# Performance work log

Measured on AMD Instinct MI355X. Metric: run time of the kernel, lower is better.

## Reference

```python
import jax, jax.numpy as jnp
import numpy as np
from jax import lax

B, T, F = 128, 100, 64
HID = [16, 32]  # encoder hidden dims; decoder uses reversed [32, 16]
K = 3


def _conv2d(x, w, b):
    # x: [N, Cin, H, W], w: [Cout, Cin, kh, kw] -> 'SAME' padding as in torch padding=k//2
    y = lax.conv_general_dilated(x, w, (1, 1), 'SAME',
                                 dimension_numbers=('NCHW', 'OIHW', 'NCHW'))
    return y + b[None, :, None, None]


def _convlstm_layer(xs, w, b, h0, c0):
    # xs: [T, B, Cin, H, W] time-major; returns hidden seq [T,B,Chid,H,W] and final (h, c)
    def step(carry, x_t):
        h, c = carry
        z = _conv2d(jnp.concatenate([x_t, h], axis=1), w, b)
        i, f, o, g = jnp.split(z, 4, axis=1)  # gate order i, f, o, g
        c2 = jax.nn.sigmoid(f) * c + jax.nn.sigmoid(i) * jnp.tanh(g)
        h2 = jax.nn.sigmoid(o) * jnp.tanh(c2)
        return (h2, c2), h2
    (hT, cT), hs = lax.scan(step, (h0, c0), xs)
    return hs, (hT, cT)


def setup_inputs() -> dict:
    key = jax.random.key(0)
    ks = jax.random.split(key, 12)
    s = 0.05
    inp = {
        'x': jax.random.normal(ks[0], (B, T, F), dtype=jnp.float32),
        # encoder layer 0: in=1+16, out=4*16
        'enc_w0': jax.random.normal(ks[1], (4 * HID[0], 1 + HID[0], K, K), dtype=jnp.float32) * s,
        'enc_b0': jnp.zeros((4 * HID[0],), dtype=jnp.float32),
        # encoder layer 1: in=16+32, out=4*32
        'enc_w1': jax.random.normal(ks[2], (4 * HID[1], HID[0] + HID[1], K, K), dtype=jnp.float32) * s,
        'enc_b1': jnp.zeros((4 * HID[1],), dtype=jnp.float32),
        # decoder layer 0: hidden=32, input=32 (last encoder hidden)
        'dec_w0': jax.random.normal(ks[3], (4 * HID[1], HID[1] + HID[1], K, K), dtype=jnp.float32) * s,
        'dec_b0': jnp.zeros((4 * HID[1],), dtype=jnp.float32),
        # decoder layer 1: hidden=16, input=32
        'dec_w1': jax.random.normal(ks[4], (4 * HID[0], HID[1] + HID[0], K, K), dtype=jnp.float32) * s,
        'dec_b1': jnp.zeros((4 * HID[0],), dtype=jnp.float32),
        # final 1x1 conv: 16 -> 1
        'fc_w': jax.random.normal(ks[5], (1, HID[0], 1, 1), dtype=jnp.float32) * s,
        'fc_b': jnp.zeros((1,), dtype=jnp.float32),
    }
    return inp


def reference(x, enc_w0, enc_b0, enc_w1, enc_b1, dec_w0, dec_b0, dec_w1, dec_b1, fc_w, fc_b):
    b, t, f = x.shape
    # [b,t,f] -> [t,b,1,f,1] time-major, spatial (f,1)
    xs = jnp.transpose(x.reshape(b, t, 1, f, 1), (1, 0, 2, 3, 4))
    z16 = jnp.zeros((b, HID[0], f, 1), x.dtype)
    z32 = jnp.zeros((b, HID[1], f, 1), x.dtype)

    enc1, (h1, c1) = _convlstm_layer(xs, enc_w0, enc_b0, z16, z16)
    enc2, (h2, c2) = _convlstm_layer(enc1, enc_w1, enc_b1, z32, z32)

    # decoder initial states = encoder final states reversed
    dec1, _ = _convlstm_layer(enc2, dec_w0, dec_b0, h2, c2)
    dec2, _ = _convlstm_layer(dec1, dec_w1, dec_b1, h1, c1)  # [t,b,16,f,1]

    # final 1x1 conv applied per timestep == one batched conv over t*b
    flat = dec2.reshape(t * b, HID[0], f, 1)
    out = _conv2d(flat, fc_w, fc_b)  # [t*b,1,f,1]
    recon = jnp.transpose(out.reshape(t, b, f), (1, 0, 2))  # [b,t,f]
    return recon
```

## Files before the change

### kernel.cpp

```cpp
#include <hip/hip_runtime.h>
#include <math.h>

#define B_ 128
#define T_ 100
#define RS 72
#define RS2 40

__device__ __forceinline__ float frcp_(float x){ return __builtin_amdgcn_rcpf(x); }
__device__ __forceinline__ float fsig_(float x){ return frcp_(1.f + __expf(-x)); }
__device__ __forceinline__ float ftanh_(float x){ float e = __expf(2.f*x); return 1.f - 2.f*frcp_(e+1.f); }
__device__ __forceinline__ float gate1(float zi, float zf, float zo, float zg, float& c){
    float cc = fsig_(zf)*c + fsig_(zi)*ftanh_(zg);
    c = cc;
    return fsig_(zo)*ftanh_(cc);
}
__device__ __forceinline__ float4 ldf4(const float* p){ return *reinterpret_cast<const float4*>(p); }
__device__ __forceinline__ void stf4(float* p, float4 v){ *reinterpret_cast<float4*>(p) = v; }
__device__ __forceinline__ float2 ldf2(const float* p){ return *reinterpret_cast<const float2*>(p); }
__device__ __forceinline__ void stf2(float* p, float2 v){ *reinterpret_cast<float2*>(p) = v; }
__device__ __forceinline__ float4 add4(float4 a, float4 b){
    return make_float4(a.x+b.x, a.y+b.y, a.z+b.z, a.w+b.w);
}
__device__ __forceinline__ float4 gate4(float4 zi, float4 zf, float4 zo, float4 zg,
                                        float bi, float bf, float bo, float bg, float4& c){
    float4 h;
    h.x = gate1(zi.x+bi, zf.x+bf, zo.x+bo, zg.x+bg, c.x);
    h.y = gate1(zi.y+bi, zf.y+bf, zo.y+bo, zg.y+bg, c.y);
    h.z = gate1(zi.z+bi, zf.z+bf, zo.z+bo, zg.z+bg, c.z);
    h.w = gate1(zi.w+bi, zf.w+bf, zo.w+bo, zg.w+bg, c.w);
    return h;
}

__device__ __forceinline__ void fma4v(float w, float u0,float u1,float u2,float u3, float4& a){
    a.x = fmaf(w,u0,a.x); a.y = fmaf(w,u1,a.y);
    a.z = fmaf(w,u2,a.z); a.w = fmaf(w,u3,a.w);
}
__device__ __forceinline__ void fma2v(float w, float u0,float u1, float2& a){
    a.x = fmaf(w,u0,a.x); a.y = fmaf(w,u1,a.y);
}

template<int ROWS>
__device__ __forceinline__ void rowacc4(const float* __restrict__ rowp,
                                        const float* __restrict__ wk,
                                        float4& ai, float4& af, float4& ao, float4& ag)
{
    float  m = rowp[-1];
    float4 a = ldf4(rowp);
    float  p = rowp[4];
    float4 wa = ldf4(wk);
    float4 wb = ldf4(wk + ROWS);
    float4 wc = ldf4(wk + 2*ROWS);
    fma4v(wa.x, m,a.x,a.y,a.z, ai);  fma4v(wa.y, m,a.x,a.y,a.z, af);
    fma4v(wa.z, m,a.x,a.y,a.z, ao);  fma4v(wa.w, m,a.x,a.y,a.z, ag);
    fma4v(wb.x, a.x,a.y,a.z,a.w, ai); fma4v(wb.y, a.x,a.y,a.z,a.w, af);
    fma4v(wb.z, a.x,a.y,a.z,a.w, ao); fma4v(wb.w, a.x,a.y,a.z,a.w, ag);
    fma4v(wc.x, a.y,a.z,a.w,p, ai);  fma4v(wc.y, a.y,a.z,a.w,p, af);
    fma4v(wc.z, a.y,a.z,a.w,p, ao);  fma4v(wc.w, a.y,a.z,a.w,p, ag);
}
template<int ROWS>
__device__ __forceinline__ void rowacc2(const float* __restrict__ rowp,
                                        const float* __restrict__ wk,
                                        float2& ai, float2& af, float2& ao, float2& ag)
{
    float  m = rowp[-1];
    float2 a = *reinterpret_cast<const float2*>(rowp);
    float  p = rowp[2];
    float4 wa = ldf4(wk);
    float4 wb = ldf4(wk + ROWS);
    float4 wc = ldf4(wk + 2*ROWS);
    fma2v(wa.x, m,a.x, ai); fma2v(wa.y, m,a.x, af);
    fma2v(wa.z, m,a.x, ao); fma2v(wa.w, m,a.x, ag);
    fma2v(wb.x, a.x,a.y, ai); fma2v(wb.y, a.x,a.y, af);
    fma2v(wb.z, a.x,a.y, ao); fma2v(wb.w, a.x,a.y, ag);
    fma2v(wc.x, a.y,p, ai); fma2v(wc.y, a.y,p, af);
    fma2v(wc.z, a.y,p, ao); fma2v(wc.w, a.y,p, ag);
}
template<int ROWS>
__device__ __forceinline__ void rowacc8(const float* __restrict__ rowp,
                                        const float* __restrict__ wk,
                                        float4& i0, float4& i1, float4& f0v, float4& f1v,
                                        float4& o0, float4& o1, float4& g0, float4& g1)
{
    float  m = rowp[-1];
    float4 a = ldf4(rowp);
    float4 b = ldf4(rowp + 4);
    float  p = rowp[8];
    float4 wa = ldf4(wk);
    float4 wb = ldf4(wk + ROWS);
    float4 wc = ldf4(wk + 2*ROWS);
    fma4v(wa.x, m,a.x,a.y,a.z, i0);   fma4v(wa.x, a.w,b.x,b.y,b.z, i1);
    fma4v(wa.y, m,a.x,a.y,a.z, f0v);  fma4v(wa.y, a.w,b.x,b.y,b.z, f1v);
    fma4v(wa.z, m,a.x,a.y,a.z, o0);   fma4v(wa.z, a.w,b.x,b.y,b.z, o1);
    fma4v(wa.w, m,a.x,a.y,a.z, g0);   fma4v(wa.w, a.w,b.x,b.y,b.z, g1);
    fma4v(wb.x, a.x,a.y,a.z,a.w, i0); fma4v(wb.x, b.x,b.y,b.z,b.w, i1);
    fma4v(wb.y, a.x,a.y,a.z,a.w, f0v);fma4v(wb.y, b.x,b.y,b.z,b.w, f1v);
    fma4v(wb.z, a.x,a.y,a.z,a.w, o0); fma4v(wb.z, b.x,b.y,b.z,b.w, o1);
    fma4v(wb.w, a.x,a.y,a.z,a.w, g0); fma4v(wb.w, b.x,b.y,b.z,b.w, g1);
    fma4v(wc.x, a.y,a.z,a.w,b.x, i0); fma4v(wc.x, b.y,b.z,b.w,p, i1);
    fma4v(wc.y, a.y,a.z,a.w,b.x, f0v);fma4v(wc.y, b.y,b.z,b.w,p, f1v);
    fma4v(wc.z, a.y,a.z,a.w,b.x, o0); fma4v(wc.z, b.y,b.z,b.w,p, o1);
    fma4v(wc.w, a.y,a.z,a.w,b.x, g0); fma4v(wc.w, b.y,b.z,b.w,p, g1);
}

__global__ __launch_bounds__(512, 1) void enc_kernel(
    const float* __restrict__ x,
    const float* __restrict__ w0, const float* __restrict__ b0,
    const float* __restrict__ w1, const float* __restrict__ b1,
    float* __restrict__ seq,
    float* __restrict__ h1f, float* __restrict__ c1f,
    float* __restrict__ h2f, float* __restrict__ c2f,
    float* __restrict__ comm, int* __restrict__ flags)
{
    __shared__ float wl0[51 * 64];
    __shared__ float wl1[144 * 128];
    __shared__ float bs0[64];
    __shared__ float bs1[128];
    __shared__ float hbuf[50 * RS2];
    __shared__ float zsA[4 * 16 * 32];
    __shared__ float zsB[4 * 32 * 32];

    const int tid = threadIdx.x;
    const int b = blockIdx.x & 127;
    const int s = blockIdx.x >> 7;
    const int gofs = s << 5;
    const int kg = tid >> 8;
    const int r  = tid & 255;
    const int chB = r >> 3, f0B = (r & 7) * 4;
    const int chA = r >> 4, f0A = (r & 15) * 2;
    const int haloSlot = s ? 3 : 36;
    const int myId = (b << 1) | s;
    const int peerId = myId ^ 1;
    float* mySend = &comm[(size_t)myId * 128];
    const float* peerBuf = &comm[(size_t)peerId * 128];

    for (int idx = tid; idx < 51 * 64; idx += 512) {
        int k = idx >> 6, rr = idx & 63;
        int ch = rr >> 2, g = rr & 3;
        int ci = k / 3, d = k - ci * 3;
        wl0[idx] = w0[((g * 16 + ch) * 17 + ci) * 9 + d * 3 + 1];
    }
    for (int idx = tid; idx < 144 * 128; idx += 512) {
        int k = idx >> 7, rr = idx & 127;
        int ch = rr >> 2, g = rr & 3;
        int ci = k / 3, d = k - ci * 3;
        wl1[idx] = w1[((g * 32 + ch) * 48 + ci) * 9 + d * 3 + 1];
    }
    if (tid < 64) bs0[tid] = b0[tid];
    if (tid < 128) bs1[tid] = b1[tid];
    for (int i = tid; i < 50 * RS2; i += 512) hbuf[i] = 0.f;
    __syncthreads();

    const int xl = tid - 256;
    if (xl >= 0 && xl < 34) {
        const int gc = gofs - 1 + xl;
        const bool v = (gc >= 0) && (gc < 64);
        hbuf[0 * RS2 + 3 + xl] = v ? x[(b * T_ + 0) * 64 + gc] : 0.f;
        hbuf[1 * RS2 + 3 + xl] = v ? x[(b * T_ + 1) * 64 + gc] : 0.f;
    }
    const float biA = bs0[chA], bfA = bs0[16+chA], boA = bs0[32+chA], bgA = bs0[48+chA];
    const float biB = bs1[chB], bfB = bs1[32+chB], boB = bs1[64+chB], bgB = bs1[96+chB];
    __syncthreads();

    const float4 z4 = make_float4(0.f, 0.f, 0.f, 0.f);
    const float2 z2 = make_float2(0.f, 0.f);
    float2 c0q = z2;
    float4 c1a = z4;

    if (kg == 0) {
        float2 ai = z2, af = z2, ao = z2, ag = z2;
        rowacc2<64>(&hbuf[0 * RS2 + 4 + f0A], &wl0[chA * 4], ai, af, ao, ag);
        float2 hq;
        hq.x = gate1(ai.x + biA, af.x + bfA, ao.x + boA, ag.x + bgA, c0q.x);
        hq.y = gate1(ai.y + biA, af.y + bfA, ao.y + boA, ag.y + bgA, c0q.y);
        *reinterpret_cast<float2*>(&hbuf[(2 + chA) * RS2 + 4 + f0A]) = hq;
        if ((r & 15) == (s ? 0 : 15)) {
            const float v = s ? hq.x : hq.y;
            __hip_atomic_store((unsigned int*)&mySend[1 * 64 + 32 + chA],
                               __float_as_uint(v),
                               __ATOMIC_RELAXED, __HIP_MEMORY_SCOPE_AGENT);
        }
    }
    __syncthreads();

#pragma unroll 1
    for (int t = 0; t < T_; ++t) {
        if (tid == 0)
            __hip_atomic_store(&flags[myId], t + 1,
                               __ATOMIC_RELAXED, __HIP_MEMORY_SCOPE_AGENT);
        if (tid < 48 && (t > 0 || tid >= 32)) {
            while (__hip_atomic_load(&flags[peerId],
                                     __ATOMIC_ACQUIRE, __HIP_MEMORY_SCOPE_AGENT) < t + 1)
                __builtin_amdgcn_s_sleep(2);
            const int par = (t + 1) & 1;
            const unsigned int uv =
                __hip_atomic_load((const unsigned int*)&peerBuf[par * 64 + tid],
                                  __ATOMIC_RELAXED, __HIP_MEMORY_SCOPE_AGENT);
            const float v = __uint_as_float(uv);
            if (tid < 32) hbuf[(18 + tid) * RS2 + haloSlot] = v;
            else          hbuf[(2 + (tid - 32)) * RS2 + haloSlot] = v;
        }
        __syncthreads();

        const bool doL0 = (t + 1 < T_);
        float4 I = z4, F = z4, O = z4, G = z4;
#pragma unroll 1
        for (int j = 0; j < 24; ++j) {
            const int ci = kg * 24 + j;
            rowacc4<128>(&hbuf[(2 + ci) * RS2 + 4 + f0B],
                         &wl1[(ci * 3) * 128 + chB * 4], I, F, O, G);
        }
        float2 ai = z2, af = z2, ao = z2, ag = z2;
        if (doL0) {
            if (kg == 0) {
                rowacc2<64>(&hbuf[((t + 1) & 1) * RS2 + 4 + f0A], &wl0[chA * 4],
                            ai, af, ao, ag);
#pragma unroll 1
                for (int j = 0; j < 8; ++j)
                    rowacc2<64>(&hbuf[(2 + j) * RS2 + 4 + f0A],
                                &wl0[((1 + j) * 3) * 64 + chA * 4], ai, af, ao, ag);
            } else {
#pragma unroll 1
                for (int j = 8; j < 16; ++j)
                    rowacc2<64>(&hbuf[(2 + j) * RS2 + 4 + f0A],
                                &wl0[((1 + j) * 3) * 64 + chA * 4], ai, af, ao, ag);
            }
        }
        if (kg == 1) {
            stf4(&zsB[(0*32+chB)*32 + f0B], I);
            stf4(&zsB[(1*32+chB)*32 + f0B], F);
            stf4(&zsB[(2*32+chB)*32 + f0B], O);
            stf4(&zsB[(3*32+chB)*32 + f0B], G);
            if (doL0) {
                *reinterpret_cast<float2*>(&zsA[(0*16+chA)*32 + f0A]) = ai;
                *reinterpret_cast<float2*>(&zsA[(1*16+chA)*32 + f0A]) = af;
                *reinterpret_cast<float2*>(&zsA[(2*16+chA)*32 + f0A]) = ao;
                *reinterpret_cast<float2*>(&zsA[(3*16+chA)*32 + f0A]) = ag;
            }
            if (xl >= 0 && xl < 34 && t + 2 < T_) {
                const int gc = gofs - 1 + xl;
                hbuf[(t & 1) * RS2 + 3 + xl] =
                    (gc >= 0 && gc < 64) ? x[(b * T_ + t + 2) * 64 + gc] : 0.f;
            }
        }
        __syncthreads();
        if (kg == 0) {
            float4 zi = add4(I, ldf4(&zsB[(0*32+chB)*32 + f0B]));
            float4 zf = add4(F, ldf4(&zsB[(1*32+chB)*32 + f0B]));
            float4 zo = add4(O, ldf4(&zsB[(2*32+chB)*32 + f0B]));
            float4 zg = add4(G, ldf4(&zsB[(3*32+chB)*32 + f0B]));
            float4 hq = gate4(zi, zf, zo, zg, biB, bfB, boB, bgB, c1a);
            stf4(&hbuf[(18 + chB) * RS2 + 4 + f0B], hq);
            stf4(&seq[((size_t)t * B_ + b) * 2048 + chB * 64 + gofs + f0B], hq);
            if (doL0 && (r & 7) == (s ? 0 : 7)) {
                const float v = s ? hq.x : hq.w;
                __hip_atomic_store((unsigned int*)&mySend[(t & 1) * 64 + chB],
                                   __float_as_uint(v),
                                   __ATOMIC_RELAXED, __HIP_MEMORY_SCOPE_AGENT);
            }
            if (doL0) {
                float2 pzi = *reinterpret_cast<const float2*>(&zsA[(0*16+chA)*32 + f0A]);
                float2 pzf = *reinterpret_cast<const float2*>(&zsA[(1*16+chA)*32 + f0A]);
                float2 pzo = *reinterpret_cast<const float2*>(&zsA[(2*16+chA)*32 + f0A]);
                float2 pzg = *reinterpret_cast<const float2*>(&zsA[(3*16+chA)*32 + f0A]);
                float2 hq2;
                hq2.x = gate1(ai.x+pzi.x+biA, af.x+pzf.x+bfA, ao.x+pzo.x+boA, ag.x+pzg.x+bgA, c0q.x);
                hq2.y = gate1(ai.y+pzi.y+biA, af.y+pzf.y+bfA, ao.y+pzo.y+boA, ag.y+pzg.y+bgA, c0q.y);
                *reinterpret_cast<float2*>(&hbuf[(2 + chA) * RS2 + 4 + f0A]) = hq2;
                if ((r & 15) == (s ? 0 : 15)) {
                    const float v = s ? hq2.x : hq2.y;
                    __hip_atomic_store((unsigned int*)&mySend[(t & 1) * 64 + 32 + chA],
                                       __float_as_uint(v),
                                       __ATOMIC_RELAXED, __HIP_MEMORY_SCOPE_AGENT);
                }
            }
        }
        __syncthreads();
    }

    if (kg == 0) {
        *reinterpret_cast<float2*>(&h1f[(b * 16 + chA) * 64 + gofs + f0A]) =
            *reinterpret_cast<const float2*>(&hbuf[(2 + chA) * RS2 + 4 + f0A]);
        *reinterpret_cast<float2*>(&c1f[(b * 16 + chA) * 64 + gofs + f0A]) = c0q;
        stf4(&h2f[b * 2048 + chB * 64 + gofs + f0B],
             ldf4(&hbuf[(18 + chB) * RS2 + 4 + f0B]));
        stf4(&c2f[b * 2048 + chB * 64 + gofs + f0B], c1a);
    }
}

__global__ __launch_bounds__(256, 2) void xconv0_kernel(
    const float* __restrict__ seqIn, const float* __restrict__ w,
    float* __restrict__ zx, int t0)
{
    __shared__ float wl[96 * 128];
    __shared__ float xt[32 * RS];

    const int tid = threadIdx.x;
    const int tl = blockIdx.x / B_;
    const int b  = blockIdx.x - tl * B_;
    const int t  = t0 + tl;

    for (int idx = tid; idx < 96 * 128; idx += 256) {
        int k = idx >> 7, rr = idx & 127;
        int ch = rr >> 2, g = rr & 3;
        int ci = k / 3, d = k - ci * 3;
        wl[idx] = w[((g * 32 + ch) * 64 + ci) * 9 + d * 3 + 1];
    }
    {
        int rr = tid >> 3, j = tid & 7;
        xt[rr * RS + (j < 4 ? j : 64 + j)] = 0.f;
    }
    {
        const float* s = &seqIn[((size_t)t * B_ + b) * 2048 + tid * 8];
        float4 v0 = ldf4(s);
        float4 v1 = ldf4(s + 4);
        int ci = tid >> 3, col = (tid & 7) * 8;
        stf4(&xt[ci * RS + 4 + col], v0);
        stf4(&xt[ci * RS + 4 + col + 4], v1);
    }
    __syncthreads();

    const int ch = tid >> 3, f0 = (tid & 7) * 8;
    const float4 z4 = make_float4(0.f,0.f,0.f,0.f);
    float4 i0=z4,i1=z4,f0v=z4,f1v=z4,o0=z4,o1=z4,g0=z4,g1=z4;
#pragma unroll 1
    for (int rr = 0; rr < 32; ++rr)
        rowacc8<128>(&xt[rr * RS + 4 + f0], wl + (rr * 3) * 128 + ch * 4,
                     i0, i1, f0v, f1v, o0, o1, g0, g1);

    float* zp = &zx[(((size_t)tl * B_ + b) * 4) * 2048 + ch * 64 + f0];
    stf4(zp, i0);            stf4(zp + 4, i1);
    stf4(zp + 2048, f0v);    stf4(zp + 2048 + 4, f1v);
    stf4(zp + 4096, o0);     stf4(zp + 4096 + 4, o1);
    stf4(zp + 6144, g0);     stf4(zp + 6144 + 4, g1);
}

__global__ __launch_bounds__(512, 1) void decg(
    const float* __restrict__ w0, const float* __restrict__ b0,
    const float* __restrict__ w1, const float* __restrict__ b1,
    const float* __restrict__ zx,
    const float* __restrict__ h0in, const float* __restrict__ c0in,
    const float* __restrict__ h1in, const float* __restrict__ c1in,
    float* __restrict__ h0sv, float* __restrict__ c0sv,
    float* __restrict__ h1sv, float* __restrict__ c1sv,
    const float* __restrict__ fw, const float* __restrict__ fb,
    float* __restrict__ out,
    float* __restrict__ comm0, float* __restrict__ comm1,
    int* __restrict__ flg, int t0, int tn, int lastc)
{
    __shared__ float wl0[96 * 128];
    __shared__ float wl1[144 * 64];
    __shared__ float hp0[32 * RS2];
    __shared__ float hp1[16 * RS2];
    __shared__ float zs0[4 * 32 * 32];
    __shared__ float zs1[4 * 16 * 32];
    __shared__ float bs0[128];
    __shared__ float bs1[64];
    __shared__ float fcw[16];
    __shared__ float fcb_s;

    const int tid = threadIdx.x;
    const int b = blockIdx.x & 127;
    const int s = blockIdx.x >> 7;
    const int gofs = s << 5;
    const int haloSlot = s ? 3 : 36;
    const int bcol = s ? 31 : 32;
    const int myId = (b << 1) | s, peerId = myId ^ 1;
    float* send0 = &comm0[(size_t)myId * 64];
    const float* peer0 = &comm0[(size_t)peerId * 64];
    float* send1 = &comm1[(size_t)myId * 32];
    const float* peer1 = &comm1[(size_t)peerId * 32];

    const int kg = tid >> 8;
    const int r = tid & 255;
    const bool isD0 = (r < 128);
    const int ch0 = r >> 2, t0f = (r & 3) * 8;
    const int r1 = r - 128;
    const int ch1 = r1 >> 3, t1f = (r1 & 7) * 4;

    for (int idx = tid; idx < 96 * 128; idx += 512) {
        int k = idx >> 7, rr = idx & 127;
        int c8 = rr >> 2, g = rr & 3;
        int ci = k / 3, d = k - ci * 3;
        wl0[idx] = w0[((g * 32 + c8) * 64 + 32 + ci) * 9 + d * 3 + 1];
    }
    for (int idx = tid; idx < 144 * 64; idx += 512) {
        int k = idx >> 6, rr = idx & 63;
        int c8 = rr >> 2, g = rr & 3;
        int ci = k / 3, d = k - ci * 3;
        wl1[idx] = w1[((g * 16 + c8) * 48 + ci) * 9 + d * 3 + 1];
    }
    if (tid < 128) bs0[tid] = b0[tid];
    if (tid < 64) bs1[tid] = b1[tid];
    if (tid < 16) fcw[tid] = fw[tid];
    if (tid == 16) fcb_s = fb[0];
    for (int i = tid; i < 32 * RS2; i += 512) hp0[i] = 0.f;
    for (int i = tid; i < 16 * RS2; i += 512) hp1[i] = 0.f;
    __syncthreads();

    for (int i = tid; i < 1024; i += 512) {
        int c8 = i >> 5, f = i & 31;
        hp0[c8 * RS2 + 4 + f] = h0in[b * 2048 + c8 * 64 + gofs + f];
    }
    { int c8 = tid >> 5, f = tid & 31;
      hp1[c8 * RS2 + 4 + f] = h1in[b * 1024 + c8 * 64 + gofs + f]; }
    if (tid < 32) hp0[tid * RS2 + haloSlot] = h0in[b * 2048 + tid * 64 + bcol];
    if (tid >= 64 && tid < 80)
        hp1[(tid - 64) * RS2 + haloSlot] = h1in[b * 1024 + (tid - 64) * 64 + bcol];

    const float4 z4 = make_float4(0.f, 0.f, 0.f, 0.f);
    float4 c0a = z4, c0b = z4;
    float4 c1v = z4;
    float bi, bfv, bo, bg;
    if (isD0) { bi = bs0[ch0]; bfv = bs0[32+ch0]; bo = bs0[64+ch0]; bg = bs0[96+ch0]; }
    else      { bi = bs1[ch1]; bfv = bs1[16+ch1]; bo = bs1[32+ch1]; bg = bs1[48+ch1]; }
    if (kg == 0) {
        if (isD0) {
            c0a = ldf4(&c0in[b * 2048 + ch0 * 64 + gofs + t0f]);
            c0b = ldf4(&c0in[b * 2048 + ch0 * 64 + gofs + t0f + 4]);
        } else {
            c1v = ldf4(&c1in[b * 1024 + ch1 * 64 + gofs + t1f]);
        }
    }
    const float fcbv = fcb_s;

#pragma unroll 1
    for (int u = t0; u < t0 + tn + lastc; ++u) {
        if (tid == 0)
            __hip_atomic_store(&flg[myId], u,
                               __ATOMIC_RELAXED, __HIP_MEMORY_SCOPE_AGENT);
        if (u > t0) {
            const int par = (u - 1) & 1;
            if (tid < 32) {
                while (__hip_atomic_load(&flg[peerId],
                                         __ATOMIC_ACQUIRE, __HIP_MEMORY_SCOPE_AGENT) < u)
                    __builtin_amdgcn_s_sleep(2);
                hp0[tid * RS2 + haloSlot] = __uint_as_float(
                    __hip_atomic_load((const unsigned int*)&peer0[par * 32 + tid],
                                      __ATOMIC_RELAXED, __HIP_MEMORY_SCOPE_AGENT));
            } else if (tid >= 64 && tid < 80 && u >= 2) {
                while (__hip_atomic_load(&flg[peerId],
                                         __ATOMIC_ACQUIRE, __HIP_MEMORY_SCOPE_AGENT) < u)
                    __builtin_amdgcn_s_sleep(2);
                hp1[(tid - 64) * RS2 + haloSlot] = __uint_as_float(
                    __hip_atomic_load((const unsigned int*)&peer1[par * 16 + (tid - 64)],
                                      __ATOMIC_RELAXED, __HIP_MEMORY_SCOPE_AGENT));
            }
        }
        __syncthreads();

        const bool d0act = (u - t0 < tn);
        const bool d1act = (u >= 1);
        float4 A0=z4,A1=z4,B0=z4,B1=z4,C0=z4,C1=z4,D0=z4,D1=z4;
        float4 ai=z4, af=z4, ao=z4, ag=z4;
        float4 X0=z4,X1=z4,X2=z4,X3=z4,X4=z4,X5=z4,X6=z4,X7=z4;

        if (isD0) {
            if (d0act) {
                if (kg == 0) {
                    const float* zp = &zx[(((size_t)(u - t0) * B_ + b) * 4) * 2048
                                          + ch0 * 64 + gofs + t0f];
                    X0 = ldf4(zp);         X1 = ldf4(zp + 4);
                    X2 = ldf4(zp + 2048);  X3 = ldf4(zp + 2052);
                    X4 = ldf4(zp + 4096);  X5 = ldf4(zp + 4100);
                    X6 = ldf4(zp + 6144);  X7 = ldf4(zp + 6148);
                }
#pragma unroll 1
                for (int j = 0; j < 16; ++j) {
                    const int ci = kg * 16 + j;
                    rowacc8<128>(&hp0[ci * RS2 + 4 + t0f], &wl0[(ci * 3) * 128 + ch0 * 4],
                                 A0, A1, B0, B1, C0, C1, D0, D1);
                }
            }
            if (kg == 1 && r < 32 && u >= 2) {
                float a = fcbv;
#pragma unroll
                for (int k2 = 0; k2 < 16; ++k2)
                    a = fmaf(fcw[k2], hp1[k2 * RS2 + 4 + r], a);
                out[(b * T_ + (u - 2)) * 64 + gofs + r] = a;
            }
        } else if (d1act) {
            if (kg == 0) {
#pragma unroll 1
                for (int j = 0; j < 24; ++j)
                    rowacc4<64>(&hp0[j * RS2 + 4 + t1f], &wl1[(j * 3) * 64 + ch1 * 4],
                                ai, af, ao, ag);
            } else {
#pragma unroll 1
                for (int j = 24; j < 32; ++j)
                    rowacc4<64>(&hp0[j * RS2 + 4 + t1f], &wl1[(j * 3) * 64 + ch1 * 4],
                                ai, af, ao, ag);
#pragma unroll 1
                for (int j = 0; j < 16; ++j)
                    rowacc4<64>(&hp1[j * RS2 + 4 + t1f], &wl1[((32 + j) * 3) * 64 + ch1 * 4],
                                ai, af, ao, ag);
            }
        }
        if (kg == 1) {
            if (isD0) { if (d0act) {
                stf4(&zs0[(0*32+ch0)*32 + t0f], A0); stf4(&zs0[(0*32+ch0)*32 + t0f + 4], A1);
                stf4(&zs0[(1*32+ch0)*32 + t0f], B0); stf4(&zs0[(1*32+ch0)*32 + t0f + 4], B1);
                stf4(&zs0[(2*32+ch0)*32 + t0f], C0); stf4(&zs0[(2*32+ch0)*32 + t0f + 4], C1);
                stf4(&zs0[(3*32+ch0)*32 + t0f], D0); stf4(&zs0[(3*32+ch0)*32 + t0f + 4], D1);
            }} else { if (d1act) {
                stf4(&zs1[(0*16+ch1)*32 + t1f], ai);
                stf4(&zs1[(1*16+ch1)*32 + t1f], af);
                stf4(&zs1[(2*16+ch1)*32 + t1f], ao);
                stf4(&zs1[(3*16+ch1)*32 + t1f], ag);
            }}
        }
        __syncthreads();
        if (kg == 0) {
            if (isD0 && d0act) {
                float4 zi0 = add4(add4(A0, X0), ldf4(&zs0[(0*32+ch0)*32 + t0f]));
                float4 zi1 = add4(add4(A1, X1), ldf4(&zs0[(0*32+ch0)*32 + t0f + 4]));
                float4 zf0 = add4(add4(B0, X2), ldf4(&zs0[(1*32+ch0)*32 + t0f]));
                float4 zf1 = add4(add4(B1, X3), ldf4(&zs0[(1*32+ch0)*32 + t0f + 4]));
                float4 zo0 = add4(add4(C0, X4), ldf4(&zs0[(2*32+ch0)*32 + t0f]));
                float4 zo1 = add4(add4(C1, X5), ldf4(&zs0[(2*32+ch0)*32 + t0f + 4]));
                float4 zg0 = add4(add4(D0, X6), ldf4(&zs0[(3*32+ch0)*32 + t0f]));
                float4 zg1 = add4(add4(D1, X7), ldf4(&zs0[(3*32+ch0)*32 + t0f + 4]));
                float4 h0q0 = gate4(zi0, zf0, zo0, zg0, bi, bfv, bo, bg, c0a);
                float4 h0q1 = gate4(zi1, zf1, zo1, zg1, bi, bfv, bo, bg, c0b);
                stf4(&hp0[ch0 * RS2 + 4 + t0f], h0q0);
                stf4(&hp0[ch0 * RS2 + 4 + t0f + 4], h0q1);
                if ((r & 3) == (s ? 0 : 3)) {
                    __hip_atomic_store((unsigned int*)&send0[(u & 1) * 32 + ch0],
                                       __float_as_uint(s ? h0q0.x : h0q1.w),
                                       __ATOMIC_RELAXED, __HIP_MEMORY_SCOPE_AGENT);
                }
            } else if (!isD0 && d1act) {
                float4 zi = add4(ai, ldf4(&zs1[(0*16+ch1)*32 + t1f]));
                float4 zf = add4(af, ldf4(&zs1[(1*16+ch1)*32 + t1f]));
                float4 zo = add4(ao, ldf4(&zs1[(2*16+ch1)*32 + t1f]));
                float4 zg = add4(ag, ldf4(&zs1[(3*16+ch1)*32 + t1f]));
                float4 h1q = gate4(zi, zf, zo, zg, bi, bfv, bo, bg, c1v);
                stf4(&hp1[ch1 * RS2 + 4 + t1f], h1q);
                if ((r1 & 7) == (s ? 0 : 7)) {
                    __hip_atomic_store((unsigned int*)&send1[(u & 1) * 16 + ch1],
                                       __float_as_uint(s ? h1q.x : h1q.w),
                                       __ATOMIC_RELAXED, __HIP_MEMORY_SCOPE_AGENT);
                }
            }
        }
        __syncthreads();
    }

    if (lastc && tid < 32) {
        float a = fcbv;
#pragma unroll
        for (int k2 = 0; k2 < 16; ++k2)
            a = fmaf(fcw[k2], hp1[k2 * RS2 + 4 + tid], a);
        out[(b * T_ + (T_ - 1)) * 64 + gofs + tid] = a;
    }
    for (int i = tid; i < 1024; i += 512) {
        int c8 = i >> 5, f = i & 31;
        h0sv[b * 2048 + c8 * 64 + gofs + f] = hp0[c8 * RS2 + 4 + f];
    }
    { int c8 = tid >> 5, f = tid & 31;
      h1sv[b * 1024 + c8 * 64 + gofs + f] = hp1[c8 * RS2 + 4 + f]; }
    if (kg == 0) {
        if (isD0) {
            stf4(&c0sv[b * 2048 + ch0 * 64 + gofs + t0f], c0a);
            stf4(&c0sv[b * 2048 + ch0 * 64 + gofs + t0f + 4], c0b);
        } else {
            stf4(&c1sv[b * 1024 + ch1 * 64 + gofs + t1f], c1v);
        }
    }
}

__global__ __launch_bounds__(512, 1) void dec0_fb(
    const float* __restrict__ w, const float* __restrict__ bias,
    float* __restrict__ seq,
    const float* __restrict__ hin, const float* __restrict__ cin)
{
    __shared__ float wl[192 * 128];
    __shared__ float bs[128];
    __shared__ float xin[32 * RS];
    __shared__ float hp[32 * RS];

    const int tid = threadIdx.x;
    const int b = blockIdx.x;

    for (int idx = tid; idx < 192 * 128; idx += 512) {
        int k = idx >> 7, rr = idx & 127;
        int ch = rr >> 2, g = rr & 3;
        int ci = k / 3, d = k - ci * 3;
        wl[idx] = w[((g * 32 + ch) * 64 + ci) * 9 + d * 3 + 1];
    }
    if (tid < 128) bs[tid] = bias[tid];
    for (int i = tid; i < 32 * RS; i += 512) { xin[i] = 0.f; hp[i] = 0.f; }
    __syncthreads();
    {
        const float* hs = &hin[b * 2048 + tid * 4];
        float4 hv = ldf4(hs);
        int ci = tid >> 4, col = (tid & 15) * 4;
        stf4(&hp[ci * RS + 4 + col], hv);
    }
    const int ch = tid >> 4, f0 = (tid & 15) * 4;
    float4 cc = ldf4(&cin[b * 2048 + ch * 64 + f0]);
    const float bi = bs[ch], bf = bs[32 + ch], bo = bs[64 + ch], bg = bs[96 + ch];
    const float4 z4 = make_float4(0.f,0.f,0.f,0.f);

    float4 nx = ldf4(&seq[(size_t)b * 2048 + tid * 4]);

#pragma unroll 1
    for (int t = 0; t < T_; ++t) {
        {
            int ci = tid >> 4, col = (tid & 15) * 4;
            stf4(&xin[ci * RS + 4 + col], nx);
        }
        __syncthreads();
        if (t + 1 < T_)
            nx = ldf4(&seq[((size_t)(t + 1) * B_ + b) * 2048 + tid * 4]);
        float4 ai = z4, af = z4, ao = z4, ag = z4;
#pragma unroll 1
        for (int rr = 0; rr < 32; ++rr)
            rowacc4<128>(&xin[rr * RS + 4 + f0], wl + (rr * 3) * 128 + ch * 4, ai, af, ao, ag);
#pragma unroll 1
        for (int rr = 0; rr < 32; ++rr)
            rowacc4<128>(&hp[rr * RS + 4 + f0], wl + ((32 + rr) * 3) * 128 + ch * 4, ai, af, ao, ag);
        float4 hn = gate4(ai, af, ao, ag, bi, bf, bo, bg, cc);
        __syncthreads();
        stf4(&hp[ch * RS + 4 + f0], hn);
        stf4(&seq[((size_t)t * B_ + b) * 2048 + ch * 64 + f0], hn);
    }
}

__global__ __launch_bounds__(512, 1) void dec1_fb(
    const float* __restrict__ w, const float* __restrict__ bias,
    const float* __restrict__ seq,
    const float* __restrict__ hin, const float* __restrict__ cin,
    const float* __restrict__ fw, const float* __restrict__ fb,
    float* __restrict__ out)
{
    __shared__ float wl[144 * 64];
    __shared__ float bs[64];
    __shared__ float xin[32 * RS];
    __shared__ float hp[16 * RS];
    __shared__ float fcw[16];
    __shared__ float fcb;

    const int tid = threadIdx.x;
    const int b = blockIdx.x;

    for (int idx = tid; idx < 144 * 64; idx += 512) {
        int k = idx >> 6, rr = idx & 63;
        int ch = rr >> 2, g = rr & 3;
        int ci = k / 3, d = k - ci * 3;
        wl[idx] = w[((g * 16 + ch) * 48 + ci) * 9 + d * 3 + 1];
    }
    if (tid < 64) bs[tid] = bias[tid];
    if (tid < 16) fcw[tid] = fw[tid];
    if (tid == 16) fcb = fb[0];
    for (int i = tid; i < 32 * RS; i += 512) xin[i] = 0.f;
    for (int i = tid; i < 16 * RS; i += 512) hp[i] = 0.f;
    __syncthreads();
    {
        const float* hs = &hin[b * 1024 + tid * 2];
        float2 hv = *reinterpret_cast<const float2*>(hs);
        int ci = tid >> 5, col = (tid & 31) * 2;
        *reinterpret_cast<float2*>(&hp[ci * RS + 4 + col]) = hv;
    }
    const int ch = tid >> 5, f0 = (tid & 31) * 2;
    float2 cc = *reinterpret_cast<const float2*>(&cin[b * 1024 + ch * 64 + f0]);
    const float bi = bs[ch], bf = bs[16 + ch], bo = bs[32 + ch], bg = bs[48 + ch];
    const float2 z2 = make_float2(0.f,0.f);
    float4 nx = ldf4(&seq[(size_t)b * 2048 + tid * 4]);
    __syncthreads();

#pragma unroll 1
    for (int t = 0; t < T_; ++t) {
        {
            int ci = tid >> 4, col = (tid & 15) * 4;
            stf4(&xin[ci * RS + 4 + col], nx);
        }
        __syncthreads();
        if (t + 1 < T_)
            nx = ldf4(&seq[((size_t)(t + 1) * B_ + b) * 2048 + tid * 4]);

        float2 ai = z2, af = z2, ao = z2, ag = z2;
#pragma unroll 1
        for (int rr = 0; rr < 32; ++rr)
            rowacc2<64>(&xin[rr * RS + 4 + f0], wl + (rr * 3) * 64 + ch * 4, ai, af, ao, ag);
#pragma unroll 1
        for (int rr = 0; rr < 16; ++rr)
            rowacc2<64>(&hp[rr * RS + 4 + f0], wl + ((32 + rr) * 3) * 64 + ch * 4, ai, af, ao, ag);

        float2 hh;
        hh.x = gate1(ai.x + bi, af.x + bf, ao.x + bo, ag.x + bg, cc.x);
        hh.y = gate1(ai.y + bi, af.y + bf, ao.y + bo, ag.y + bg, cc.y);
        __syncthreads();
        *reinterpret_cast<float2*>(&hp[ch * RS + 4 + f0]) = hh;
        __syncthreads();

        if (tid < 64) {
            float a = fcb;
#pragma unroll
            for (int k2 = 0; k2 < 16; ++k2)
                a = fmaf(fcw[k2], hp[k2 * RS + 4 + tid], a);
            out[(b * T_ + t) * 64 + tid] = a;
        }
    }
}

extern "C" void kernel_launch(void* const* d_in, const int* in_sizes, int n_in,
                              void* d_out, int out_size, void* d_ws, size_t ws_size,
                              hipStream_t stream)
{
    (void)in_sizes; (void)n_in; (void)out_size;
    const float* x   = (const float*)d_in[0];
    const float* ew0 = (const float*)d_in[1];
    const float* eb0 = (const float*)d_in[2];
    const float* ew1 = (const float*)d_in[3];
    const float* eb1 = (const float*)d_in[4];
    const float* dw0 = (const float*)d_in[5];
    const float* db0 = (const float*)d_in[6];
    const float* dw1 = (const float*)d_in[7];
    const float* db1 = (const float*)d_in[8];
    const float* fw  = (const float*)d_in[9];
    const float* fb  = (const float*)d_in[10];
    float* out = (float*)d_out;

    float* ws  = (float*)d_ws;
    size_t off = 0;
    float* seq = ws + off; off += (size_t)T_ * B_ * 2048;
    float* h1f = ws + off; off += (size_t)B_ * 1024;
    float* c1f = ws + off; off += (size_t)B_ * 1024;
    float* h2f = ws + off; off += (size_t)B_ * 2048;
    float* c2f = ws + off; off += (size_t)B_ * 2048;
    float* hd0 = ws + off; off += (size_t)B_ * 2048;
    float* cd0 = ws + off; off += (size_t)B_ * 2048;
    float* hd1 = ws + off; off += (size_t)B_ * 1024;
    float* cd1 = ws + off; off += (size_t)B_ * 1024;
    float* comm = ws + off; off += 32768 + 16384 + 8192;
    int*   flg  = (int*)(ws + off); off += 1024;
    float* zx  = ws + off;

    float* commD0 = comm + 32768;
    float* commD1 = comm + 32768 + 16384;

    size_t availf = (ws_size / 4 > off) ? (ws_size / 4 - off) : 0;
    int TC = 0;
    if      (availf >= (size_t)100 * B_ * 8192) TC = 100;
    else if (availf >= (size_t)50  * B_ * 8192) TC = 50;
    else if (availf >= (size_t)25  * B_ * 8192) TC = 25;
    else if (availf >= (size_t)10  * B_ * 8192) TC = 10;

    hipMemsetAsync(flg, 0, 512 * sizeof(int), stream);
    enc_kernel<<<256, 512, 0, stream>>>(x, ew0, eb0, ew1, eb1, seq,
                                        h1f, c1f, h2f, c2f, comm, flg);

    if (TC > 0) {
        for (int t0 = 0; t0 < T_; t0 += TC) {
            int tn = (t0 + TC <= T_) ? TC : (T_ - t0);
            int lastc = (t0 + tn >= T_) ? 1 : 0;
            xconv0_kernel<<<tn * B_, 256, 0, stream>>>(seq, dw0, zx, t0);
            decg<<<256, 512, 0, stream>>>(
                dw0, db0, dw1, db1, zx,
                t0 == 0 ? h2f : hd0, t0 == 0 ? c2f : cd0,
                t0 == 0 ? h1f : hd1, t0 == 0 ? c1f : cd1,
                hd0, cd0, hd1, cd1,
                fw, fb, out, commD0, commD1, flg + 256, t0, tn, lastc);
        }
    } else {
        dec0_fb<<<B_, 512, 0, stream>>>(dw0, db0, seq, h2f, c2f);
        dec1_fb<<<B_, 512, 0, stream>>>(dw1, db1, seq, h1f, c1f, fw, fb, out);
    }
}
```

Before: 2.066 ms.

## Repartition encoder layer-1 and decoder layer-1 convs into four-way input-channel split-K

The encoder's second ConvLSTM layer previously split its 48 input rows between two 256-thread halves, each thread computing 4 columns. It now splits them four ways across 128-thread groups, each thread computing 8 columns with rowacc8. Three partial sums go to a larger shared buffer and group 0 reduces them and applies the gates. The decoder layer-1 work gets the same treatment: its 48 input rows are split evenly into four 12-row chunks instead of an uneven 24/24 split. The aim is to shorten the serial per-timestep critical path and improve per-thread reuse, at the cost of more shared memory, extra reduction loads and higher register pressure.

```diff
diff --git a/kernel.cpp b/kernel.cpp
--- a/kernel.cpp
+++ b/kernel.cpp
@@ -117,7 +117,7 @@
     __shared__ float bs1[128];
     __shared__ float hbuf[50 * RS2];
     __shared__ float zsA[4 * 16 * 32];
-    __shared__ float zsB[4 * 32 * 32];
+    __shared__ float zsB3[3 * 4096];
 
     const int tid = threadIdx.x;
     const int b = blockIdx.x & 127;
@@ -125,7 +125,9 @@
     const int gofs = s << 5;
     const int kg = tid >> 8;
     const int r  = tid & 255;
-    const int chB = r >> 3, f0B = (r & 7) * 4;
+    const int g  = tid >> 7;
+    const int rg = tid & 127;
+    const int chB = rg >> 2, f0B = (rg & 3) * 8;
     const int chA = r >> 4, f0A = (r & 15) * 2;
     const int haloSlot = s ? 3 : 36;
     const int myId = (b << 1) | s;
@@ -135,15 +137,15 @@
 
     for (int idx = tid; idx < 51 * 64; idx += 512) {
         int k = idx >> 6, rr = idx & 63;
-        int ch = rr >> 2, g = rr & 3;
+        int ch = rr >> 2, gg = rr & 3;
         int ci = k / 3, d = k - ci * 3;
-        wl0[idx] = w0[((g * 16 + ch) * 17 + ci) * 9 + d * 3 + 1];
+        wl0[idx] = w0[((gg * 16 + ch) * 17 + ci) * 9 + d * 3 + 1];
     }
     for (int idx = tid; idx < 144 * 128; idx += 512) {
         int k = idx >> 7, rr = idx & 127;
-        int ch = rr >> 2, g = rr & 3;
+        int ch = rr >> 2, gg = rr & 3;
         int ci = k / 3, d = k - ci * 3;
-        wl1[idx] = w1[((g * 32 + ch) * 48 + ci) * 9 + d * 3 + 1];
+        wl1[idx] = w1[((gg * 32 + ch) * 48 + ci) * 9 + d * 3 + 1];
     }
     if (tid < 64) bs0[tid] = b0[tid];
     if (tid < 128) bs1[tid] = b1[tid];
@@ -164,7 +166,7 @@
     const float4 z4 = make_float4(0.f, 0.f, 0.f, 0.f);
     const float2 z2 = make_float2(0.f, 0.f);
     float2 c0q = z2;
-    float4 c1a = z4;
+    float4 c1a = z4, c1b = z4;
 
     if (kg == 0) {
         float2 ai = z2, af = z2, ao = z2, ag = z2;
@@ -202,12 +204,13 @@
         __syncthreads();
 
         const bool doL0 = (t + 1 < T_);
-        float4 I = z4, F = z4, O = z4, G = z4;
-#pragma unroll 1
-        for (int j = 0; j < 24; ++j) {
-            const int ci = kg * 24 + j;
-            rowacc4<128>(&hbuf[(2 + ci) * RS2 + 4 + f0B],
-                         &wl1[(ci * 3) * 128 + chB * 4], I, F, O, G);
+        float4 I0=z4,I1=z4,F0=z4,F1=z4,O0=z4,O1=z4,G0=z4,G1=z4;
+#pragma unroll 1
+        for (int j = 0; j < 12; ++j) {
+            const int ci = 12 * g + j;
+            rowacc8<128>(&hbuf[(2 + ci) * RS2 + 4 + f0B],
+                         &wl1[(ci * 3) * 128 + chB * 4],
+                         I0, I1, F0, F1, O0, O1, G0, G1);
         }
         float2 ai = z2, af = z2, ao = z2, ag = z2;
         if (doL0) {
@@ -225,11 +228,14 @@
                                 &wl0[((1 + j) * 3) * 64 + chA * 4], ai, af, ao, ag);
             }
         }
+        if (g != 0) {
+            float* zp = &zsB3[(g - 1) * 4096];
+            stf4(&zp[(0*32+chB)*32 + f0B], I0); stf4(&zp[(0*32+chB)*32 + f0B + 4], I1);
+            stf4(&zp[(1*32+chB)*32 + f0B], F0); stf4(&zp[(1*32+chB)*32 + f0B + 4], F1);
+            stf4(&zp[(2*32+chB)*32 + f0B], O0); stf4(&zp[(2*32+chB)*32 + f0B + 4], O1);
+            stf4(&zp[(3*32+chB)*32 + f0B], G0); stf4(&zp[(3*32+chB)*32 + f0B + 4], G1);
+        }
         if (kg == 1) {
-            stf4(&zsB[(0*32+chB)*32 + f0B], I);
-            stf4(&zsB[(1*32+chB)*32 + f0B], F);
-            stf4(&zsB[(2*32+chB)*32 + f0B], O);
-            stf4(&zsB[(3*32+chB)*32 + f0B], G);
             if (doL0) {
                 *reinterpret_cast<float2*>(&zsA[(0*16+chA)*32 + f0A]) = ai;
                 *reinterpret_cast<float2*>(&zsA[(1*16+chA)*32 + f0A]) = af;
@@ -243,35 +249,47 @@
             }
         }
         __syncthreads();
-        if (kg == 0) {
-            float4 zi = add4(I, ldf4(&zsB[(0*32+chB)*32 + f0B]));
-            float4 zf = add4(F, ldf4(&zsB[(1*32+chB)*32 + f0B]));
-            float4 zo = add4(O, ldf4(&zsB[(2*32+chB)*32 + f0B]));
-            float4 zg = add4(G, ldf4(&zsB[(3*32+chB)*32 + f0B]));
-            float4 hq = gate4(zi, zf, zo, zg, biB, bfB, boB, bgB, c1a);
-            stf4(&hbuf[(18 + chB) * RS2 + 4 + f0B], hq);
-            stf4(&seq[((size_t)t * B_ + b) * 2048 + chB * 64 + gofs + f0B], hq);
-            if (doL0 && (r & 7) == (s ? 0 : 7)) {
-                const float v = s ? hq.x : hq.w;
+        if (g == 0) {
+            const float* s0 = &zsB3[0];
+            const float* s1 = &zsB3[4096];
+            const float* s2 = &zsB3[8192];
+            const int oI = (0*32+chB)*32 + f0B, oF = (1*32+chB)*32 + f0B;
+            const int oO = (2*32+chB)*32 + f0B, oG = (3*32+chB)*32 + f0B;
+            float4 zi0 = add4(add4(I0, ldf4(&s0[oI])), add4(ldf4(&s1[oI]), ldf4(&s2[oI])));
+            float4 zi1 = add4(add4(I1, ldf4(&s0[oI+4])), add4(ldf4(&s1[oI+4]), ldf4(&s2[oI+4])));
+            float4 zf0 = add4(add4(F0, ldf4(&s0[oF])), add4(ldf4(&s1[oF]), ldf4(&s2[oF])));
+            float4 zf1 = add4(add4(F1, ldf4(&s0[oF+4])), add4(ldf4(&s1[oF+4]), ldf4(&s2[oF+4])));
+            float4 zo0 = add4(add4(O0, ldf4(&s0[oO])), add4(ldf4(&s1[oO]), ldf4(&s2[oO])));
+            float4 zo1 = add4(add4(O1, ldf4(&s0[oO+4])), add4(ldf4(&s1[oO+4]), ldf4(&s2[oO+4])));
+            float4 zg0 = add4(add4(G0, ldf4(&s0[oG])), add4(ldf4(&s1[oG]), ldf4(&s2[oG])));
+            float4 zg1 = add4(add4(G1, ldf4(&s0[oG+4])), add4(ldf4(&s1[oG+4]), ldf4(&s2[oG+4])));
+            float4 hq0 = gate4(zi0, zf0, zo0, zg0, biB, bfB, boB, bgB, c1a);
+            float4 hq1 = gate4(zi1, zf1, zo1, zg1, biB, bfB, boB, bgB, c1b);
+            stf4(&hbuf[(18 + chB) * RS2 + 4 + f0B], hq0);
+            stf4(&hbuf[(18 + chB) * RS2 + 4 + f0B + 4], hq1);
+            float* sp = &seq[((size_t)t * B_ + b) * 2048 + chB * 64 + gofs + f0B];
+            stf4(sp, hq0); stf4(sp + 4, hq1);
+            if (doL0 && (rg & 3) == (s ? 0 : 3)) {
+                const float v = s ? hq0.x : hq1.w;
                 __hip_atomic_store((unsigned int*)&mySend[(t & 1) * 64 + chB],
                                    __float_as_uint(v),
                                    __ATOMIC_RELAXED, __HIP_MEMORY_SCOPE_AGENT);
             }
-            if (doL0) {
-                float2 pzi = *reinterpret_cast<const float2*>(&zsA[(0*16+chA)*32 + f0A]);
-                float2 pzf = *reinterpret_cast<const float2*>(&zsA[(1*16+chA)*32 + f0A]);
-                float2 pzo = *reinterpret_cast<const float2*>(&zsA[(2*16+chA)*32 + f0A]);
-                float2 pzg = *reinterpret_cast<const float2*>(&zsA[(3*16+chA)*32 + f0A]);
-                float2 hq2;
-                hq2.x = gate1(ai.x+pzi.x+biA, af.x+pzf.x+bfA, ao.x+pzo.x+boA, ag.x+pzg.x+bgA, c0q.x);
-                hq2.y = gate1(ai.y+pzi.y+biA, af.y+pzf.y+bfA, ao.y+pzo.y+boA, ag.y+pzg.y+bgA, c0q.y);
-                *reinterpret_cast<float2*>(&hbuf[(2 + chA) * RS2 + 4 + f0A]) = hq2;
-                if ((r & 15) == (s ? 0 : 15)) {
-                    const float v = s ? hq2.x : hq2.y;
-                    __hip_atomic_store((unsigned int*)&mySend[(t & 1) * 64 + 32 + chA],
-                                       __float_as_uint(v),
-                                       __ATOMIC_RELAXED, __HIP_MEMORY_SCOPE_AGENT);
-                }
+        }
+        if (kg == 0 && doL0) {
+            float2 pzi = *reinterpret_cast<const float2*>(&zsA[(0*16+chA)*32 + f0A]);
+            float2 pzf = *reinterpret_cast<const float2*>(&zsA[(1*16+chA)*32 + f0A]);
+            float2 pzo = *reinterpret_cast<const float2*>(&zsA[(2*16+chA)*32 + f0A]);
+            float2 pzg = *reinterpret_cast<const float2*>(&zsA[(3*16+chA)*32 + f0A]);
+            float2 hq2;
+            hq2.x = gate1(ai.x+pzi.x+biA, af.x+pzf.x+bfA, ao.x+pzo.x+boA, ag.x+pzg.x+bgA, c0q.x);
+            hq2.y = gate1(ai.y+pzi.y+biA, af.y+pzf.y+bfA, ao.y+pzo.y+boA, ag.y+pzg.y+bgA, c0q.y);
+            *reinterpret_cast<float2*>(&hbuf[(2 + chA) * RS2 + 4 + f0A]) = hq2;
+            if ((r & 15) == (s ? 0 : 15)) {
+                const float v = s ? hq2.x : hq2.y;
+                __hip_atomic_store((unsigned int*)&mySend[(t & 1) * 64 + 32 + chA],
+                                   __float_as_uint(v),
+                                   __ATOMIC_RELAXED, __HIP_MEMORY_SCOPE_AGENT);
             }
         }
         __syncthreads();
@@ -281,9 +299,13 @@
         *reinterpret_cast<float2*>(&h1f[(b * 16 + chA) * 64 + gofs + f0A]) =
             *reinterpret_cast<const float2*>(&hbuf[(2 + chA) * RS2 + 4 + f0A]);
         *reinterpret_cast<float2*>(&c1f[(b * 16 + chA) * 64 + gofs + f0A]) = c0q;
-        stf4(&h2f[b * 2048 + chB * 64 + gofs + f0B],
-             ldf4(&hbuf[(18 + chB) * RS2 + 4 + f0B]));
-        stf4(&c2f[b * 2048 + chB * 64 + gofs + f0B], c1a);
+    }
+    if (g == 0) {
+        float* hp2 = &h2f[b * 2048 + chB * 64 + gofs + f0B];
+        stf4(hp2,     ldf4(&hbuf[(18 + chB) * RS2 + 4 + f0B]));
+        stf4(hp2 + 4, ldf4(&hbuf[(18 + chB) * RS2 + 4 + f0B + 4]));
+        float* cp2 = &c2f[b * 2048 + chB * 64 + gofs + f0B];
+        stf4(cp2, c1a); stf4(cp2 + 4, c1b);
     }
 }
 
@@ -352,7 +374,7 @@
     __shared__ float hp0[32 * RS2];
     __shared__ float hp1[16 * RS2];
     __shared__ float zs0[4 * 32 * 32];
-    __shared__ float zs1[4 * 16 * 32];
+    __shared__ float zs1_3[3 * 2048];
     __shared__ float bs0[128];
     __shared__ float bs1[64];
     __shared__ float fcw[16];
@@ -374,8 +396,10 @@
     const int r = tid & 255;
     const bool isD0 = (r < 128);
     const int ch0 = r >> 2, t0f = (r & 3) * 8;
-    const int r1 = r - 128;
-    const int ch1 = r1 >> 3, t1f = (r1 & 7) * 4;
+    const int q1 = r - 128;
+    const int d1g = kg * 2 + ((q1 >> 6) & 1);
+    const int rg1 = q1 & 63;
+    const int ch1 = rg1 >> 2, t1f = (rg1 & 3) * 8;
 
     for (int idx = tid; idx < 96 * 128; idx += 512) {
         int k = idx >> 7, rr = idx & 127;
@@ -409,17 +433,17 @@
 
     const float4 z4 = make_float4(0.f, 0.f, 0.f, 0.f);
     float4 c0a = z4, c0b = z4;
-    float4 c1v = z4;
+    float4 c1a_ = z4, c1b_ = z4;
     float bi, bfv, bo, bg;
     if (isD0) { bi = bs0[ch0]; bfv = bs0[32+ch0]; bo = bs0[64+ch0]; bg = bs0[96+ch0]; }
     else      { bi = bs1[ch1]; bfv = bs1[16+ch1]; bo = bs1[32+ch1]; bg = bs1[48+ch1]; }
-    if (kg == 0) {
-        if (isD0) {
-            c0a = ldf4(&c0in[b * 2048 + ch0 * 64 + gofs + t0f]);
-            c0b = ldf4(&c0in[b * 2048 + ch0 * 64 + gofs + t0f + 4]);
-        } else {
-            c1v = ldf4(&c1in[b * 1024 + ch1 * 64 + gofs + t1f]);
-        }
+    if (kg == 0 && isD0) {
+        c0a = ldf4(&c0in[b * 2048 + ch0 * 64 + gofs + t0f]);
+        c0b = ldf4(&c0in[b * 2048 + ch0 * 64 + gofs + t0f + 4]);
+    }
+    if (!isD0 && d1g == 0) {
+        c1a_ = ldf4(&c1in[b * 1024 + ch1 * 64 + gofs + t1f]);
+        c1b_ = ldf4(&c1in[b * 1024 + ch1 * 64 + gofs + t1f + 4]);
     }
     const float fcbv = fcb_s;
 
@@ -451,7 +475,6 @@
         const bool d0act = (u - t0 < tn);
         const bool d1act = (u >= 1);
         float4 A0=z4,A1=z4,B0=z4,B1=z4,C0=z4,C1=z4,D0=z4,D1=z4;
-        float4 ai=z4, af=z4, ao=z4, ag=z4;
         float4 X0=z4,X1=z4,X2=z4,X3=z4,X4=z4,X5=z4,X6=z4,X7=z4;
 
         if (isD0) {
@@ -479,67 +502,73 @@
                 out[(b * T_ + (u - 2)) * 64 + gofs + r] = a;
             }
         } else if (d1act) {
-            if (kg == 0) {
-#pragma unroll 1
-                for (int j = 0; j < 24; ++j)
-                    rowacc4<64>(&hp0[j * RS2 + 4 + t1f], &wl1[(j * 3) * 64 + ch1 * 4],
-                                ai, af, ao, ag);
-            } else {
-#pragma unroll 1
-                for (int j = 24; j < 32; ++j)
-                    rowacc4<64>(&hp0[j * RS2 + 4 + t1f], &wl1[(j * 3) * 64 + ch1 * 4],
-                                ai, af, ao, ag);
-#pragma unroll 1
-                for (int j = 0; j < 16; ++j)
-                    rowacc4<64>(&hp1[j * RS2 + 4 + t1f], &wl1[((32 + j) * 3) * 64 + ch1 * 4],
-                                ai, af, ao, ag);
-            }
-        }
-        if (kg == 1) {
-            if (isD0) { if (d0act) {
+            const int rlo = 12 * d1g, rhi = rlo + 12;
+            const int xhi = rhi < 32 ? rhi : 32;
+            const int hlo = rlo > 32 ? rlo : 32;
+#pragma unroll 1
+            for (int rr = rlo; rr < xhi; ++rr)
+                rowacc8<64>(&hp0[rr * RS2 + 4 + t1f], &wl1[(rr * 3) * 64 + ch1 * 4],
+                            A0, A1, B0, B1, C0, C1, D0, D1);
+#pragma unroll 1
+            for (int rr = hlo; rr < rhi; ++rr)
+                rowacc8<64>(&hp1[(rr - 32) * RS2 + 4 + t1f], &wl1[(rr * 3) * 64 + ch1 * 4],
+                            A0, A1, B0, B1, C0, C1, D0, D1);
+        }
+        if (isD0) {
+            if (kg == 1 && d0act) {
                 stf4(&zs0[(0*32+ch0)*32 + t0f], A0); stf4(&zs0[(0*32+ch0)*32 + t0f + 4], A1);
                 stf4(&zs0[(1*32+ch0)*32 + t0f], B0); stf4(&zs0[(1*32+ch0)*32 + t0f + 4], B1);
                 stf4(&zs0[(2*32+ch0)*32 + t0f], C0); stf4(&zs0[(2*32+ch0)*32 + t0f + 4], C1);
                 stf4(&zs0[(3*32+ch0)*32 + t0f], D0); stf4(&zs0[(3*32+ch0)*32 + t0f + 4], D1);
-            }} else { if (d1act) {
-                stf4(&zs1[(0*16+ch1)*32 + t1f], ai);
-                stf4(&zs1[(1*16+ch1)*32 + t1f], af);
-                stf4(&zs1[(2*16+ch1)*32 + t1f], ao);
-                stf4(&zs1[(3*16+ch1)*32 + t1f], ag);
-            }}
-        }
-        __syncthreads();
-        if (kg == 0) {
-            if (isD0 && d0act) {
-                float4 zi0 = add4(add4(A0, X0), ldf4(&zs0[(0*32+ch0)*32 + t0f]));
-                float4 zi1 = add4(add4(A1, X1), ldf4(&zs0[(0*32+ch0)*32 + t0f + 4]));
-                float4 zf0 = add4(add4(B0, X2), ldf4(&zs0[(1*32+ch0)*32 + t0f]));
-                float4 zf1 = add4(add4(B1, X3), ldf4(&zs0[(1*32+ch0)*32 + t0f + 4]));
-                float4 zo0 = add4(add4(C0, X4), ldf4(&zs0[(2*32+ch0)*32 + t0f]));
-                float4 zo1 = add4(add4(C1, X5), ldf4(&zs0[(2*32+ch0)*32 + t0f + 4]));
-                float4 zg0 = add4(add4(D0, X6), ldf4(&zs0[(3*32+ch0)*32 + t0f]));
-                float4 zg1 = add4(add4(D1, X7), ldf4(&zs0[(3*32+ch0)*32 + t0f + 4]));
-                float4 h0q0 = gate4(zi0, zf0, zo0, zg0, bi, bfv, bo, bg, c0a);
-                float4 h0q1 = gate4(zi1, zf1, zo1, zg1, bi, bfv, bo, bg, c0b);
-                stf4(&hp0[ch0 * RS2 + 4 + t0f], h0q0);
-                stf4(&hp0[ch0 * RS2 + 4 + t0f + 4], h0q1);
-                if ((r & 3) == (s ? 0 : 3)) {
-                    __hip_atomic_store((unsigned int*)&send0[(u & 1) * 32 + ch0],
-                                       __float_as_uint(s ? h0q0.x : h0q1.w),
-                                       __ATOMIC_RELAXED, __HIP_MEMORY_SCOPE_AGENT);
-                }
-            } else if (!isD0 && d1act) {
-                float4 zi = add4(ai, ldf4(&zs1[(0*16+ch1)*32 + t1f]));
-                float4 zf = add4(af, ldf4(&zs1[(1*16+ch1)*32 + t1f]));
-                float4 zo = add4(ao, ldf4(&zs1[(2*16+ch1)*32 + t1f]));
-                float4 zg = add4(ag, ldf4(&zs1[(3*16+ch1)*32 + t1f]));
-                float4 h1q = gate4(zi, zf, zo, zg, bi, bfv, bo, bg, c1v);
-                stf4(&hp1[ch1 * RS2 + 4 + t1f], h1q);
-                if ((r1 & 7) == (s ? 0 : 7)) {
-                    __hip_atomic_store((unsigned int*)&send1[(u & 1) * 16 + ch1],
-                                       __float_as_uint(s ? h1q.x : h1q.w),
-                                       __ATOMIC_RELAXED, __HIP_MEMORY_SCOPE_AGENT);
-                }
+            }
+        } else if (d1g != 0 && d1act) {
+            float* zp = &zs1_3[(d1g - 1) * 2048];
+            stf4(&zp[(0*16+ch1)*32 + t1f], A0); stf4(&zp[(0*16+ch1)*32 + t1f + 4], A1);
+            stf4(&zp[(1*16+ch1)*32 + t1f], B0); stf4(&zp[(1*16+ch1)*32 + t1f + 4], B1);
+            stf4(&zp[(2*16+ch1)*32 + t1f], C0); stf4(&zp[(2*16+ch1)*32 + t1f + 4], C1);
+            stf4(&zp[(3*16+ch1)*32 + t1f], D0); stf4(&zp[(3*16+ch1)*32 + t1f + 4], D1);
+        }
+        __syncthreads();
+        if (isD0 && kg == 0 && d0act) {
+            float4 zi0 = add4(add4(A0, X0), ldf4(&zs0[(0*32+ch0)*32 + t0f]));
+            float4 zi1 = add4(add4(A1, X1), ldf4(&zs0[(0*32+ch0)*32 + t0f + 4]));
+            float4 zf0 = add4(add4(B0, X2), ldf4(&zs0[(1*32+ch0)*32 + t0f]));
+            float4 zf1 = add4(add4(B1, X3), ldf4(&zs0[(1*32+ch0)*32 + t0f + 4]));
+            float4 zo0 = add4(add4(C0, X4), ldf4(&zs0[(2*32+ch0)*32 + t0f]));
+            float4 zo1 = add4(add4(C1, X5), ldf4(&zs0[(2*32+ch0)*32 + t0f + 4]));
+            float4 zg0 = add4(add4(D0, X6), ldf4(&zs0[(3*32+ch0)*32 + t0f]));
+            float4 zg1 = add4(add4(D1, X7), ldf4(&zs0[(3*32+ch0)*32 + t0f + 4]));
+            float4 h0q0 = gate4(zi0, zf0, zo0, zg0, bi, bfv, bo, bg, c0a);
+            float4 h0q1 = gate4(zi1, zf1, zo1, zg1, bi, bfv, bo, bg, c0b);
+            stf4(&hp0[ch0 * RS2 + 4 + t0f], h0q0);
+            stf4(&hp0[ch0 * RS2 + 4 + t0f + 4], h0q1);
+            if ((r & 3) == (s ? 0 : 3)) {
+                __hip_atomic_store((unsigned int*)&send0[(u & 1) * 32 + ch0],
+                                   __float_as_uint(s ? h0q0.x : h0q1.w),
+                                   __ATOMIC_RELAXED, __HIP_MEMORY_SCOPE_AGENT);
+            }
+        } else if (!isD0 && d1g == 0 && d1act) {
+            const float* s0 = &zs1_3[0];
+            const float* s1 = &zs1_3[2048];
+            const float* s2 = &zs1_3[4096];
+            const int oI = (0*16+ch1)*32 + t1f, oF = (1*16+ch1)*32 + t1f;
+            const int oO = (2*16+ch1)*32 + t1f, oG = (3*16+ch1)*32 + t1f;
+            float4 zi0 = add4(add4(A0, ldf4(&s0[oI])), add4(ldf4(&s1[oI]), ldf4(&s2[oI])));
+            float4 zi1 = add4(add4(A1, ldf4(&s0[oI+4])), add4(ldf4(&s1[oI+4]), ldf4(&s2[oI+4])));
+            float4 zf0 = add4(add4(B0, ldf4(&s0[oF])), add4(ldf4(&s1[oF]), ldf4(&s2[oF])));
+            float4 zf1 = add4(add4(B1, ldf4(&s0[oF+4])), add4(ldf4(&s1[oF+4]), ldf4(&s2[oF+4])));
+            float4 zo0 = add4(add4(C0, ldf4(&s0[oO])), add4(ldf4(&s1[oO]), ldf4(&s2[oO])));
+            float4 zo1 = add4(add4(C1, ldf4(&s0[oO+4])), add4(ldf4(&s1[oO+4]), ldf4(&s2[oO+4])));
+            float4 zg0 = add4(add4(D0, ldf4(&s0[oG])), add4(ldf4(&s1[oG]), ldf4(&s2[oG])));
+            float4 zg1 = add4(add4(D1, ldf4(&s0[oG+4])), add4(ldf4(&s1[oG+4]), ldf4(&s2[oG+4])));
+            float4 h1q0 = gate4(zi0, zf0, zo0, zg0, bi, bfv, bo, bg, c1a_);
+            float4 h1q1 = gate4(zi1, zf1, zo1, zg1, bi, bfv, bo, bg, c1b_);
+            stf4(&hp1[ch1 * RS2 + 4 + t1f], h1q0);
+            stf4(&hp1[ch1 * RS2 + 4 + t1f + 4], h1q1);
+            if ((rg1 & 3) == (s ? 0 : 3)) {
+                __hip_atomic_store((unsigned int*)&send1[(u & 1) * 16 + ch1],
+                                   __float_as_uint(s ? h1q0.x : h1q1.w),
+                                   __ATOMIC_RELAXED, __HIP_MEMORY_SCOPE_AGENT);
             }
         }
         __syncthreads();
@@ -558,13 +587,13 @@
     }
     { int c8 = tid >> 5, f = tid & 31;
       h1sv[b * 1024 + c8 * 64 + gofs + f] = hp1[c8 * RS2 + 4 + f]; }
-    if (kg == 0) {
-        if (isD0) {
-            stf4(&c0sv[b * 2048 + ch0 * 64 + gofs + t0f], c0a);
-            stf4(&c0sv[b * 2048 + ch0 * 64 + gofs + t0f + 4], c0b);
-        } else {
-            stf4(&c1sv[b * 1024 + ch1 * 64 + gofs + t1f], c1v);
-        }
+    if (isD0 && kg == 0) {
+        stf4(&c0sv[b * 2048 + ch0 * 64 + gofs + t0f], c0a);
+        stf4(&c0sv[b * 2048 + ch0 * 64 + gofs + t0f + 4], c0b);
+    }
+    if (!isD0 && d1g == 0) {
+        stf4(&c1sv[b * 1024 + ch1 * 64 + gofs + t1f], c1a_);
+        stf4(&c1sv[b * 1024 + ch1 * 64 + gofs + t1f + 4], c1b_);
     }
 }
 
```

Measured after the change: 2.114 ms. 1.02x slower.
